# Performance work log

Hardware: AMD Instinct MI355X
Metric: run time of the kernel (lower is better)

## Reference

```python
import jax, jax.numpy as jnp
import numpy as np
import math

B, N, D = 4, 4096, 256


def setup_inputs() -> dict:
    key = jax.random.key(0)
    k0, k1, k2, k3 = jax.random.split(key, 4)
    # kaiming-uniform-like init for the square weight matrices
    bound = math.sqrt(6.0 / D)
    return {
        "x": jax.random.normal(k0, (B, N, D), dtype=jnp.float32),
        "Wq": jax.random.uniform(k1, (D, D), dtype=jnp.float32, minval=-bound, maxval=bound),
        "Wk": jax.random.uniform(k2, (D, D), dtype=jnp.float32, minval=-bound, maxval=bound),
        "Wv": jax.random.uniform(k3, (D, D), dtype=jnp.float32, minval=-bound, maxval=bound),
    }


def reference(x, Wq, Wk, Wv):
    # x: [B, N, D]; W*: [D, D]
    q = x @ Wq.T
    k = x @ Wk.T
    v = x @ Wv.T
    n = x.shape[1]
    d_k = x.shape[2]
    # mask = triu(ones, diagonal=1): 1 strictly above the diagonal.
    # (1 - mask) is 1 on and below the diagonal, so those positions get -1e10
    # (faithful to the original: it masks the diagonal and past, keeps future).
    mask = jnp.triu(jnp.ones((n, n), dtype=x.dtype), k=1)
    scale = jnp.asarray(1.0 / math.sqrt(d_k), dtype=x.dtype)
    s = (jnp.einsum('bnd,bmd->bnm', q, k) - (1.0 - mask) * 1e10) * scale
    # Faithful quirk: softmax over dim=1 (the query/row axis), not the last axis.
    s = jax.nn.softmax(s, axis=1)
    return jnp.einsum('bnm,bmd->bnd', s, v)
```

## Files before the change

### kernel.cpp

```cpp
#include <hip/hip_runtime.h>
#include <hip/hip_bf16.h>


typedef float f32x4 __attribute__((ext_vector_type(4)));
typedef __bf16 bf16x8 __attribute__((ext_vector_type(8)));
typedef __bf16 bf16x4 __attribute__((ext_vector_type(4)));

#define MFMA16(a, b, c) __builtin_amdgcn_mfma_f32_16x16x32_bf16((a), (b), (c), 0, 0, 0)

constexpr int SEQ = 4096;
constexpr int DIM = 256;

__device__ __forceinline__ void gl16(const __bf16* g, __bf16* l) {
  __builtin_amdgcn_global_load_lds((const __attribute__((address_space(1))) void*)g,
                                   (__attribute__((address_space(3))) void*)l, 16, 0, 0);
}

__global__ void k_prep(const float* __restrict__ Wq, const float* __restrict__ Wk,
                       const float* __restrict__ Wv, __bf16* __restrict__ Wb,
                       float* __restrict__ colsum) {
  int i = blockIdx.x * 256 + threadIdx.x;
  if (i < 3 * 65536) {
    const float* src = (i < 65536) ? Wq : (i < 131072 ? Wk : Wv);
    Wb[i] = (__bf16)src[i & 65535];
  }
  if (i < 4 * SEQ) colsum[i] = 0.f;
}

__global__ __launch_bounds__(256, 2) void k_qkv(const float* __restrict__ x,
                                                const __bf16* __restrict__ Wb,
                                                __bf16* __restrict__ Qb,
                                                __bf16* __restrict__ Kb,
                                                __bf16* __restrict__ Vb) {
  __shared__ __bf16 wsh[64][264];
  const int t = threadIdx.x, lane = t & 63, w = t >> 6;
  const int ln = lane & 15, quad = lane >> 4, q8 = quad * 8;
  const int i0 = blockIdx.x * 64;
  bf16x8 xa[8];
#pragma unroll
  for (int kf = 0; kf < 8; ++kf) {
    const float* src = &x[(size_t)(i0 + w * 16 + ln) * DIM + kf * 32 + q8];
    float4 v0 = *(const float4*)&src[0];
    float4 v1 = *(const float4*)&src[4];
    xa[kf] = bf16x8{(__bf16)v0.x, (__bf16)v0.y, (__bf16)v0.z, (__bf16)v0.w,
                    (__bf16)v1.x, (__bf16)v1.y, (__bf16)v1.z, (__bf16)v1.w};
  }
  for (int zj = 0; zj < 12; ++zj) {
    const int z = zj >> 2, j0 = (zj & 3) * 64;
    const __bf16* W = Wb + z * 65536 + j0 * 256;
    bf16x8 stg[8];
#pragma unroll
    for (int i = 0; i < 8; ++i) stg[i] = *(const bf16x8*)&W[(t + i * 256) * 8];
    __syncthreads();
#pragma unroll
    for (int i = 0; i < 8; ++i)
      *(bf16x8*)&wsh[(t >> 5) + i * 8][(t & 31) * 8] = stg[i];
    __syncthreads();
    f32x4 acc[4] = {};
#pragma unroll
    for (int kf = 0; kf < 8; ++kf) {
      bf16x8 bb[4];
#pragma unroll
      for (int tj = 0; tj < 4; ++tj)
        bb[tj] = *(bf16x8*)&wsh[tj * 16 + ln][kf * 32 + q8];
#pragma unroll
      for (int tj = 0; tj < 4; ++tj) acc[tj] = MFMA16(xa[kf], bb[tj], acc[tj]);
    }
    __bf16* Out = (z == 0) ? Qb : (z == 1 ? Kb : Vb);
#pragma unroll
    for (int tj = 0; tj < 4; ++tj)
#pragma unroll
      for (int r = 0; r < 4; ++r) {
        int row = i0 + w * 16 + quad * 4 + r;
        int col = j0 + tj * 16 + ln;
        Out[(size_t)row * DIM + col] = (__bf16)acc[tj][r];
      }
  }
}

__global__ __launch_bounds__(256, 2) void k_colsum(const __bf16* __restrict__ Qb,
                                                   const __bf16* __restrict__ Kb,
                                                   float* __restrict__ colsum) {
  __shared__ __bf16 qsh[2 * 64 * 256];
  const int t = threadIdx.x, lane = t & 63, w = t >> 6;
  const int ln = lane & 15, quad = lane >> 4, q8 = quad * 8;
  const int bid = blockIdx.x;
  const int b = (bid & 7) >> 1;
  const int i = ((bid >> 3) << 1) | (bid & 1);
  const int round = i >> 6, k = i & 63;
  const int mt = (round & 1) ? 63 - k : k;
  const int s = round;
  const int m0 = mt * 64;
  const __bf16* Qp = Qb + (size_t)b * SEQ * DIM;
  const __bf16* Kp = Kb + (size_t)b * SEQ * DIM;
  bf16x8 kb[8];
#pragma unroll
  for (int kf = 0; kf < 8; ++kf)
    kb[kf] = *(const bf16x8*)&Kp[(size_t)(m0 + w * 16 + ln) * DIM + kf * 32 + q8];
  auto stageq = [&](int ncv, int buf) {
    const __bf16* src = Qp + (size_t)ncv * 16384;
#pragma unroll
    for (int i2 = 0; i2 < 8; ++i2) {
      int sl = t + i2 * 256;
      int row = sl >> 5, g = sl & 31;
      gl16(&src[row * 256 + ((g ^ (row & 15)) << 3)], &qsh[buf * 16384 + sl * 8]);
    }
  };
  float csum = 0.f;
  int nc = s, cur = 0;
  if (nc <= mt) stageq(nc, 0);
  for (; nc <= mt; nc += 4, cur ^= 1) {
    __syncthreads();
    if (nc + 4 <= mt) stageq(nc + 4, cur ^ 1);
    f32x4 acc[4] = {};
#pragma unroll
    for (int kf = 0; kf < 8; ++kf) {
#pragma unroll
      for (int tn = 0; tn < 4; ++tn) {
        int row = tn * 16 + ln;
        bf16x8 af = *(const bf16x8*)&qsh[cur * 16384 + row * 256 +
                                         (((kf * 4 + quad) ^ ln) << 3)];
        acc[tn] = MFMA16(af, kb[kf], acc[tn]);
      }
    }
    const int m_g = m0 + w * 16 + ln;
#pragma unroll
    for (int tn = 0; tn < 4; ++tn)
#pragma unroll
      for (int r = 0; r < 4; ++r) {
        int n_g = nc * 64 + tn * 16 + quad * 4 + r;
        if (n_g < m_g) csum += __expf(acc[tn][r] * 0.0625f);
      }
  }
  csum += __shfl_xor(csum, 16);
  csum += __shfl_xor(csum, 32);
  if (quad == 0) atomicAdd(&colsum[b * SEQ + m0 + w * 16 + ln], csum);
}

__global__ void k_vpt(const __bf16* __restrict__ Vb, const float* __restrict__ colsum,
                      __bf16* __restrict__ VpT) {
  __shared__ __bf16 tile[64][72];
  const int t = threadIdx.x;
  const int b = blockIdx.z;
  const int m0 = blockIdx.x * 64, d0 = blockIdx.y * 64;
  {
    int row = t >> 2, part = t & 3;
    float cs = colsum[b * SEQ + m0 + row];
    float inv = (m0 + row == 0) ? (1.0f / 4096.0f) : (1.0f / cs);
#pragma unroll
    for (int i = 0; i < 2; ++i) {
      int c = part * 2 + i;
      bf16x8 v = *(const bf16x8*)&Vb[(size_t)(b * SEQ + m0 + row) * DIM + d0 + c * 8];
      bf16x8 o;
#pragma unroll
      for (int j = 0; j < 8; ++j) o[j] = (__bf16)((float)v[j] * inv);
      *(bf16x8*)&tile[row][c * 8] = o;
    }
  }
  __syncthreads();
  {
    int row = t >> 2, part = t & 3;
#pragma unroll
    for (int i = 0; i < 2; ++i) {
      int c = part * 2 + i;
      bf16x8 o;
#pragma unroll
      for (int j = 0; j < 8; ++j) o[j] = tile[c * 8 + j][row];
      *(bf16x8*)&VpT[(size_t)((b * 64 + blockIdx.x) * 256 + d0 + row) * 64 + c * 8] = o;
    }
  }
}

__global__ __launch_bounds__(256, 2) void k_attn(const __bf16* __restrict__ Qb,
                                                 const __bf16* __restrict__ Kb,
                                                 const __bf16* __restrict__ Vt_blk,
                                                 const __bf16* __restrict__ Vb,
                                                 __bf16* __restrict__ opart,
                                                 float* __restrict__ out_f32,
                                                 int nsplit, int fuse) {
  __shared__ __bf16 ksh[64 * 256];
  __shared__ __bf16 vsm[256 * 64];
  __shared__ __bf16 ps[64 * 72];
  const int t = threadIdx.x, lane = t & 63, w = t >> 6;
  const int ln = lane & 15, quad = lane >> 4, q8 = quad * 8;
  const int wn = w & 1;
  const int wm = w >> 1;
  const int bid = blockIdx.x;
  const int b = (bid & 7) >> 1;
  const int i = ((bid >> 3) << 1) | (bid & 1);
  int nt, s;
  if (nsplit == 1) {
    nt = i & 63; s = 0;
  } else {
    int round = i >> 6, k = i & 63;
    nt = (round & 1) ? 63 - k : k;
    s = round;
  }
  const int n0 = nt * 64;
  const __bf16* Qp = Qb + (size_t)b * SEQ * DIM;
  const __bf16* Kp = Kb + (size_t)b * SEQ * DIM;
  const __bf16* Vt = Vt_blk + (size_t)b * SEQ * DIM;
  bf16x8 qf[2][8];
#pragma unroll
  for (int tn = 0; tn < 2; ++tn)
#pragma unroll
    for (int kf = 0; kf < 8; ++kf)
      qf[tn][kf] = *(const bf16x8*)&Qp[(size_t)(n0 + wn * 32 + tn * 16 + ln) * DIM + kf * 32 + q8];
  auto stageK = [&](int msv) {
    const __bf16* kp = Kp + (size_t)msv * 16384;
#pragma unroll
    for (int i2 = 0; i2 < 8; ++i2) {
      int sl = t + i2 * 256;
      int row = sl >> 5, g = sl & 31;
      gl16(&kp[row * 256 + ((g ^ (row & 15)) << 3)], &ksh[sl * 8]);
    }
  };
  auto stageV = [&](int msv) {
    const __bf16* vp = Vt + (size_t)msv * 16384;
#pragma unroll
    for (int i2 = 0; i2 < 8; ++i2) {
      int sl = t + i2 * 256;
      int d = sl >> 3, g = sl & 7;
      gl16(&vp[d * 64 + ((g ^ (d & 7)) << 3)], &vsm[sl * 8]);
    }
  };
  f32x4 accO[2][8] = {};
  const int msEnd = nt;
  int ms = 63 - s;
  if (ms >= msEnd) { stageK(ms); stageV(ms); }
  __syncthreads();
  for (; ms >= msEnd; ms -= nsplit) {
    const int msn = ms - nsplit;
    f32x4 accS[2][2] = {};
#pragma unroll
    for (int kf = 0; kf < 8; ++kf) {
      bf16x8 bb[2];
#pragma unroll
      for (int tm = 0; tm < 2; ++tm) {
        int row = wm * 32 + tm * 16 + ln;
        bb[tm] = *(const bf16x8*)&ksh[row * 256 + (((kf * 4 + quad) ^ ln) << 3)];
      }
#pragma unroll
      for (int tn = 0; tn < 2; ++tn)
#pragma unroll
        for (int tm = 0; tm < 2; ++tm)
          accS[tn][tm] = MFMA16(qf[tn][kf], bb[tm], accS[tn][tm]);
    }
    __syncthreads();
    if (msn >= msEnd) stageK(msn);
#pragma unroll
    for (int tn = 0; tn < 2; ++tn)
#pragma unroll
      for (int tm = 0; tm < 2; ++tm) {
        int ml = wm * 32 + tm * 16 + ln;
        int m_g = ms * 64 + ml;
#pragma unroll
        for (int r = 0; r < 4; ++r) {
          int nl = wn * 32 + tn * 16 + quad * 4 + r;
          float e = (n0 + nl >= m_g) ? 0.f : __expf(accS[tn][tm][r] * 0.0625f);
          ps[nl * 72 + ml] = (__bf16)e;
        }
      }
    __syncthreads();
#pragma unroll
    for (int kf = 0; kf < 2; ++kf) {
      bf16x8 aa[2];
#pragma unroll
      for (int tn = 0; tn < 2; ++tn)
        aa[tn] = *(const bf16x8*)&ps[(wn * 32 + tn * 16 + ln) * 72 + kf * 32 + q8];
#pragma unroll
      for (int td = 0; td < 8; ++td) {
        int d = wm * 128 + td * 16 + ln;
        bf16x8 bb = *(const bf16x8*)&vsm[d * 64 + (((kf * 4 + quad) ^ (ln & 7)) << 3)];
#pragma unroll
        for (int tn = 0; tn < 2; ++tn) accO[tn][td] = MFMA16(aa[tn], bb, accO[tn][td]);
      }
    }
    __syncthreads();
    if (msn >= msEnd) stageV(msn);
    __syncthreads();
  }
  if (fuse) {
    const __bf16* V0 = Vb + (size_t)b * SEQ * DIM;
    float* Op = out_f32 + (size_t)b * SEQ * DIM;
#pragma unroll
    for (int tn = 0; tn < 2; ++tn)
#pragma unroll
      for (int td = 0; td < 8; ++td) {
        int col = wm * 128 + td * 16 + ln;
        float c0 = (float)V0[col] * (1.0f / 4096.0f);
#pragma unroll
        for (int r = 0; r < 4; ++r) {
          int row = n0 + wn * 32 + tn * 16 + quad * 4 + r;
          Op[(size_t)row * DIM + col] = accO[tn][td][r] + c0;
        }
      }
  } else {
    __bf16* P = opart + (size_t)s * (4u << 20) + ((size_t)b << 20);
#pragma unroll
    for (int tn = 0; tn < 2; ++tn)
#pragma unroll
      for (int td = 0; td < 8; ++td) {
        int col = wm * 128 + td * 16 + ln;
#pragma unroll
        for (int r = 0; r < 4; ++r) {
          int row = n0 + wn * 32 + tn * 16 + quad * 4 + r;
          P[(size_t)row * DIM + col] = (__bf16)accO[tn][td][r];
        }
      }
  }
}

__global__ void k_final(const __bf16* __restrict__ opart, const __bf16* __restrict__ Vb,
                        float* __restrict__ out, int nsplit) {
  const size_t base = ((size_t)blockIdx.x * 256 + threadIdx.x) * 8;
  const int b = (int)(base >> 20);
  const int d0 = (int)(base & 255);
  float sum[8] = {};
  for (int s = 0; s < nsplit; ++s) {
    bf16x8 v = *(const bf16x8*)&opart[(size_t)s * (4u << 20) + base];
#pragma unroll
    for (int j = 0; j < 8; ++j) sum[j] += (float)v[j];
  }
  bf16x8 v0 = *(const bf16x8*)&Vb[((size_t)b << 20) + d0];
  float4 o0, o1;
  o0.x = sum[0] + (float)v0[0] * (1.0f / 4096.0f);
  o0.y = sum[1] + (float)v0[1] * (1.0f / 4096.0f);
  o0.z = sum[2] + (float)v0[2] * (1.0f / 4096.0f);
  o0.w = sum[3] + (float)v0[3] * (1.0f / 4096.0f);
  o1.x = sum[4] + (float)v0[4] * (1.0f / 4096.0f);
  o1.y = sum[5] + (float)v0[5] * (1.0f / 4096.0f);
  o1.z = sum[6] + (float)v0[6] * (1.0f / 4096.0f);
  o1.w = sum[7] + (float)v0[7] * (1.0f / 4096.0f);
  *(float4*)&out[base] = o0;
  *(float4*)&out[base + 4] = o1;
}

extern "C" void kernel_launch(void* const* d_in, const int* in_sizes, int n_in,
                              void* d_out, int out_size, void* d_ws, size_t ws_size,
                              hipStream_t stream) {
  const float* x = (const float*)d_in[0];
  const float* Wq = (const float*)d_in[1];
  const float* Wk = (const float*)d_in[2];
  const float* Wv = (const float*)d_in[3];
  float* out = (float*)d_out;
  char* ws = (char*)d_ws;
  __bf16* Qb = (__bf16*)(ws);
  __bf16* Kb = (__bf16*)(ws + (8u << 20));
  __bf16* Vb = (__bf16*)(ws + (16u << 20));
  __bf16* VpT = (__bf16*)(ws + (24u << 20));
  float* colsum = (float*)(ws + (32u << 20));
  __bf16* Wb = (__bf16*)(ws + (32u << 20) + (1u << 16));
  const size_t base = (32u << 20) + (1u << 16) + (384u << 10);
  __bf16* opart = (__bf16*)(ws + base);
  int nsplit = 1;
  if (ws_size >= base + 4u * (8u << 20)) nsplit = 4;
  else if (ws_size >= base + 2u * (8u << 20)) nsplit = 2;
  const int fuse = (nsplit == 1);

  k_prep<<<dim3(768), dim3(256), 0, stream>>>(Wq, Wk, Wv, Wb, colsum);
  k_qkv<<<dim3(256), dim3(256), 0, stream>>>(x, Wb, Qb, Kb, Vb);
  k_colsum<<<dim3(1024), dim3(256), 0, stream>>>(Qb, Kb, colsum);
  k_vpt<<<dim3(64, 4, 4), dim3(256), 0, stream>>>(Vb, colsum, VpT);
  k_attn<<<dim3(256 * nsplit), dim3(256), 0, stream>>>(Qb, Kb, VpT, Vb, opart, out,
                                                       nsplit, fuse);
  if (!fuse)
    k_final<<<dim3(2048), dim3(256), 0, stream>>>(opart, Vb, out, nsplit);
}
```

Baseline: 204.9 us.

## Replace strided split-K attention with chunked triangular tiles and atomic output accumulation

The attention grid is repartitioned into 1152 blocks, each covering a query tile and one 8-wide chunk of key tiles in the causal triangle. This replaces the round-robin nsplit scheme that wrote bf16 partials and needed a separate reduction kernel. The output is initialised with the V-row-0 bias term in a new kernel, and blocks then add their partial sums with float atomics, removing the partial buffer traffic and balancing work per block. The S tile is also computed transposed so each lane can pack four probabilities into one vector LDS store. The cost is atomic contention on the output, and each block reloads Q while covering fewer key tiles.

```diff
diff --git a/kernel.cpp b/kernel.cpp
--- a/kernel.cpp
+++ b/kernel.cpp
@@ -171,13 +171,28 @@
   }
 }
 
+__global__ void k_oinit(const __bf16* __restrict__ Vb, float* __restrict__ out) {
+  const size_t base = ((size_t)blockIdx.x * 256 + threadIdx.x) * 8;
+  const int b = (int)(base >> 20);
+  const int d0 = (int)(base & 255);
+  bf16x8 v0 = *(const bf16x8*)&Vb[((size_t)b << 20) + d0];
+  float4 o0, o1;
+  o0.x = (float)v0[0] * (1.0f / 4096.0f);
+  o0.y = (float)v0[1] * (1.0f / 4096.0f);
+  o0.z = (float)v0[2] * (1.0f / 4096.0f);
+  o0.w = (float)v0[3] * (1.0f / 4096.0f);
+  o1.x = (float)v0[4] * (1.0f / 4096.0f);
+  o1.y = (float)v0[5] * (1.0f / 4096.0f);
+  o1.z = (float)v0[6] * (1.0f / 4096.0f);
+  o1.w = (float)v0[7] * (1.0f / 4096.0f);
+  *(float4*)&out[base] = o0;
+  *(float4*)&out[base + 4] = o1;
+}
+
 __global__ __launch_bounds__(256, 2) void k_attn(const __bf16* __restrict__ Qb,
                                                  const __bf16* __restrict__ Kb,
                                                  const __bf16* __restrict__ Vt_blk,
-                                                 const __bf16* __restrict__ Vb,
-                                                 __bf16* __restrict__ opart,
-                                                 float* __restrict__ out_f32,
-                                                 int nsplit, int fuse) {
+                                                 float* __restrict__ out) {
   __shared__ __bf16 ksh[64 * 256];
   __shared__ __bf16 vsm[256 * 64];
   __shared__ __bf16 ps[64 * 72];
@@ -187,15 +202,12 @@
   const int wm = w >> 1;
   const int bid = blockIdx.x;
   const int b = (bid & 7) >> 1;
-  const int i = ((bid >> 3) << 1) | (bid & 1);
-  int nt, s;
-  if (nsplit == 1) {
-    nt = i & 63; s = 0;
-  } else {
-    int round = i >> 6, k = i & 63;
-    nt = (round & 1) ? 63 - k : k;
-    s = round;
-  }
+  int rem = ((bid >> 3) << 1) | (bid & 1);
+  int c = 7;
+  while (rem >= 8 * c + 8) { rem -= 8 * c + 8; --c; }
+  const int nt = rem;
+  const int lo = (nt > 8 * c) ? nt : 8 * c;
+  const int hi = 8 * c + 7;
   const int n0 = nt * 64;
   const __bf16* Qp = Qb + (size_t)b * SEQ * DIM;
   const __bf16* Kp = Kb + (size_t)b * SEQ * DIM;
@@ -225,41 +237,41 @@
     }
   };
   f32x4 accO[2][8] = {};
-  const int msEnd = nt;
-  int ms = 63 - s;
-  if (ms >= msEnd) { stageK(ms); stageV(ms); }
+  stageK(hi);
+  stageV(hi);
   __syncthreads();
-  for (; ms >= msEnd; ms -= nsplit) {
-    const int msn = ms - nsplit;
-    f32x4 accS[2][2] = {};
+  for (int ms = hi; ms >= lo; --ms) {
+    const int msn = ms - 1;
+    f32x4 accST[2][2] = {};
 #pragma unroll
     for (int kf = 0; kf < 8; ++kf) {
-      bf16x8 bb[2];
+      bf16x8 af[2];
 #pragma unroll
       for (int tm = 0; tm < 2; ++tm) {
         int row = wm * 32 + tm * 16 + ln;
-        bb[tm] = *(const bf16x8*)&ksh[row * 256 + (((kf * 4 + quad) ^ ln) << 3)];
-      }
-#pragma unroll
-      for (int tn = 0; tn < 2; ++tn)
-#pragma unroll
-        for (int tm = 0; tm < 2; ++tm)
-          accS[tn][tm] = MFMA16(qf[tn][kf], bb[tm], accS[tn][tm]);
-    }
-    __syncthreads();
-    if (msn >= msEnd) stageK(msn);
-#pragma unroll
-    for (int tn = 0; tn < 2; ++tn)
-#pragma unroll
-      for (int tm = 0; tm < 2; ++tm) {
-        int ml = wm * 32 + tm * 16 + ln;
-        int m_g = ms * 64 + ml;
+        af[tm] = *(const bf16x8*)&ksh[row * 256 + (((kf * 4 + quad) ^ ln) << 3)];
+      }
+#pragma unroll
+      for (int tm = 0; tm < 2; ++tm)
+#pragma unroll
+        for (int tn = 0; tn < 2; ++tn)
+          accST[tm][tn] = MFMA16(af[tm], qf[tn][kf], accST[tm][tn]);
+    }
+    __syncthreads();
+    if (msn >= lo) stageK(msn);
+#pragma unroll
+    for (int tm = 0; tm < 2; ++tm)
+#pragma unroll
+      for (int tn = 0; tn < 2; ++tn) {
+        int n_g = n0 + wn * 32 + tn * 16 + ln;
+        int mbase = ms * 64 + wm * 32 + tm * 16 + quad * 4;
+        bf16x4 pk;
 #pragma unroll
         for (int r = 0; r < 4; ++r) {
-          int nl = wn * 32 + tn * 16 + quad * 4 + r;
-          float e = (n0 + nl >= m_g) ? 0.f : __expf(accS[tn][tm][r] * 0.0625f);
-          ps[nl * 72 + ml] = (__bf16)e;
+          float e = (n_g < mbase + r) ? __expf(accST[tm][tn][r] * 0.0625f) : 0.f;
+          pk[r] = (__bf16)e;
         }
+        *(bf16x4*)&ps[(wn * 32 + tn * 16 + ln) * 72 + wm * 32 + tm * 16 + quad * 4] = pk;
       }
     __syncthreads();
 #pragma unroll
@@ -277,63 +289,21 @@
       }
     }
     __syncthreads();
-    if (msn >= msEnd) stageV(msn);
-    __syncthreads();
-  }
-  if (fuse) {
-    const __bf16* V0 = Vb + (size_t)b * SEQ * DIM;
-    float* Op = out_f32 + (size_t)b * SEQ * DIM;
-#pragma unroll
-    for (int tn = 0; tn < 2; ++tn)
-#pragma unroll
-      for (int td = 0; td < 8; ++td) {
-        int col = wm * 128 + td * 16 + ln;
-        float c0 = (float)V0[col] * (1.0f / 4096.0f);
-#pragma unroll
-        for (int r = 0; r < 4; ++r) {
-          int row = n0 + wn * 32 + tn * 16 + quad * 4 + r;
-          Op[(size_t)row * DIM + col] = accO[tn][td][r] + c0;
-        }
-      }
-  } else {
-    __bf16* P = opart + (size_t)s * (4u << 20) + ((size_t)b << 20);
-#pragma unroll
-    for (int tn = 0; tn < 2; ++tn)
-#pragma unroll
-      for (int td = 0; td < 8; ++td) {
-        int col = wm * 128 + td * 16 + ln;
-#pragma unroll
-        for (int r = 0; r < 4; ++r) {
-          int row = n0 + wn * 32 + tn * 16 + quad * 4 + r;
-          P[(size_t)row * DIM + col] = (__bf16)accO[tn][td][r];
-        }
-      }
-  }
-}
-
-__global__ void k_final(const __bf16* __restrict__ opart, const __bf16* __restrict__ Vb,
-                        float* __restrict__ out, int nsplit) {
-  const size_t base = ((size_t)blockIdx.x * 256 + threadIdx.x) * 8;
-  const int b = (int)(base >> 20);
-  const int d0 = (int)(base & 255);
-  float sum[8] = {};
-  for (int s = 0; s < nsplit; ++s) {
-    bf16x8 v = *(const bf16x8*)&opart[(size_t)s * (4u << 20) + base];
-#pragma unroll
-    for (int j = 0; j < 8; ++j) sum[j] += (float)v[j];
-  }
-  bf16x8 v0 = *(const bf16x8*)&Vb[((size_t)b << 20) + d0];
-  float4 o0, o1;
-  o0.x = sum[0] + (float)v0[0] * (1.0f / 4096.0f);
-  o0.y = sum[1] + (float)v0[1] * (1.0f / 4096.0f);
-  o0.z = sum[2] + (float)v0[2] * (1.0f / 4096.0f);
-  o0.w = sum[3] + (float)v0[3] * (1.0f / 4096.0f);
-  o1.x = sum[4] + (float)v0[4] * (1.0f / 4096.0f);
-  o1.y = sum[5] + (float)v0[5] * (1.0f / 4096.0f);
-  o1.z = sum[6] + (float)v0[6] * (1.0f / 4096.0f);
-  o1.w = sum[7] + (float)v0[7] * (1.0f / 4096.0f);
-  *(float4*)&out[base] = o0;
-  *(float4*)&out[base + 4] = o1;
+    if (msn >= lo) stageV(msn);
+    __syncthreads();
+  }
+  float* Op = out + ((size_t)b << 20);
+#pragma unroll
+  for (int tn = 0; tn < 2; ++tn)
+#pragma unroll
+    for (int td = 0; td < 8; ++td) {
+      int col = wm * 128 + td * 16 + ln;
+#pragma unroll
+      for (int r = 0; r < 4; ++r) {
+        int row = n0 + wn * 32 + tn * 16 + quad * 4 + r;
+        unsafeAtomicAdd(&Op[(size_t)row * DIM + col], accO[tn][td][r]);
+      }
+    }
 }
 
 extern "C" void kernel_launch(void* const* d_in, const int* in_sizes, int n_in,
@@ -351,19 +321,11 @@
   __bf16* VpT = (__bf16*)(ws + (24u << 20));
   float* colsum = (float*)(ws + (32u << 20));
   __bf16* Wb = (__bf16*)(ws + (32u << 20) + (1u << 16));
-  const size_t base = (32u << 20) + (1u << 16) + (384u << 10);
-  __bf16* opart = (__bf16*)(ws + base);
-  int nsplit = 1;
-  if (ws_size >= base + 4u * (8u << 20)) nsplit = 4;
-  else if (ws_size >= base + 2u * (8u << 20)) nsplit = 2;
-  const int fuse = (nsplit == 1);
 
   k_prep<<<dim3(768), dim3(256), 0, stream>>>(Wq, Wk, Wv, Wb, colsum);
   k_qkv<<<dim3(256), dim3(256), 0, stream>>>(x, Wb, Qb, Kb, Vb);
   k_colsum<<<dim3(1024), dim3(256), 0, stream>>>(Qb, Kb, colsum);
   k_vpt<<<dim3(64, 4, 4), dim3(256), 0, stream>>>(Vb, colsum, VpT);
-  k_attn<<<dim3(256 * nsplit), dim3(256), 0, stream>>>(Qb, Kb, VpT, Vb, opart, out,
-                                                       nsplit, fuse);
-  if (!fuse)
-    k_final<<<dim3(2048), dim3(256), 0, stream>>>(opart, Vb, out, nsplit);
-}
+  k_oinit<<<dim3(2048), dim3(256), 0, stream>>>(Vb, out);
+  k_attn<<<dim3(1152), dim3(256), 0, stream>>>(Qb, Kb, VpT, out);
+}
```

Result: slower. 228.6 us (+11.5%).
